# Kernel optimization log

Hardware: AMD Instinct MI355X
Metric: run time of the kernel (lower is better)

## Reference

```python
import jax, jax.numpy as jnp
import numpy as np

K = 2
BN_EPS = 1e-5


def setup_inputs() -> dict:
    key = jax.random.key(0)
    k1, k2, k3 = jax.random.split(key, 3)
    B, C, H, W, D, O = 4, 128, 32, 32, 32, 128
    x = jax.random.normal(k1, (B, C, H, W, D), dtype=jnp.float32)
    conv_w = jax.random.normal(k2, (O, 2 * C), dtype=jnp.float32) * 0.02  # 1x1x1 conv kernel
    conv_b = jax.random.normal(k3, (O,), dtype=jnp.float32) * 0.02
    bn_gamma = jnp.ones((O,), dtype=jnp.float32)
    bn_beta = jnp.zeros((O,), dtype=jnp.float32)
    return {"x": x, "conv_w": conv_w, "conv_b": conv_b,
            "bn_gamma": bn_gamma, "bn_beta": bn_beta}


def _axis_running_max(x, x_j, axis, dim):
    # torch.cat([x[..., -i:], x[..., :-i]], axis) == jnp.roll(x, i, axis)
    shifts = jnp.arange(K, dim, K)

    def step(carry, s):
        diff = x - jnp.roll(x, s, axis=axis)
        return jnp.maximum(carry, diff), None

    x_j, _ = jax.lax.scan(step, x_j, shifts)
    return x_j


def reference(x, conv_w, conv_b, bn_gamma, bn_beta):
    B, C, H, W, D = x.shape
    x_j = jnp.zeros_like(x)
    x_j = _axis_running_max(x, x_j, 2, H)
    x_j = _axis_running_max(x, x_j, 3, W)
    x_j = _axis_running_max(x, x_j, 4, D)
    x_j = jax.lax.stop_gradient(x_j)  # original detaches every x_j update

    xc = jnp.concatenate([x, x_j], axis=1)  # [B, 2C, H, W, D]
    # 1x1x1 Conv3d == per-voxel channel GEMM
    y = jnp.einsum('bchwd,oc->bohwd', xc, conv_w) + conv_b[None, :, None, None, None]

    # BatchNorm3d, training mode (batch statistics over B,H,W,D)
    mean = y.mean(axis=(0, 2, 3, 4), keepdims=True)
    var = ((y - mean) ** 2).mean(axis=(0, 2, 3, 4), keepdims=True)
    yn = (y - mean) * jax.lax.rsqrt(var + BN_EPS)
    yn = yn * bn_gamma[None, :, None, None, None] + bn_beta[None, :, None, None, None]

    # torch nn.GELU default is exact erf form
    return jax.nn.gelu(yn, approximate=False)
```

## Files before the change

kernel.cpp:

```cpp
#include <hip/hip_runtime.h>
#include <hip/hip_bf16.h>

#define BB 4
#define CCH 128
#define C2 256
#define OO 128
#define NVOX 32768
#define NTOT (BB*NVOX)
#define NGB 1024

typedef __attribute__((ext_vector_type(4))) float f32x4;
typedef __attribute__((ext_vector_type(8))) short s16x8;
typedef __attribute__((ext_vector_type(4))) unsigned int u32x4;
typedef unsigned int u32;
typedef unsigned short u16;

#define SWZ(r) ((((r)>>3) ^ (r)) & 7)

__device__ __forceinline__ float bf2f(short s){
  union { u32 i; float f; } cv; cv.i = ((u32)(u16)s) << 16; return cv.f;
}
__device__ __forceinline__ short f2bf(float f){
  union { __hip_bfloat16 h; short s; } cv; cv.h = __float2bfloat16(f); return cv.s;
}
__device__ __forceinline__ u32 pack2(float a, float b){
  return ((u32)(u16)f2bf(a)) | (((u32)(u16)f2bf(b)) << 16);
}
__device__ __forceinline__ float ulo(u32 r){
  union { u32 i; float f; } cv; cv.i = r << 16; return cv.f;
}
__device__ __forceinline__ float uhi(u32 r){
  union { u32 i; float f; } cv; cv.i = r & 0xffff0000u; return cv.f;
}
__device__ __forceinline__ float bfr(float f){ return bf2f(f2bf(f)); }

__global__ __launch_bounds__(256) void k_convw(const float* __restrict__ w, short* __restrict__ wb){
  int i = blockIdx.x*256 + threadIdx.x;
  wb[i] = f2bf(w[i]);
}

__global__ __launch_bounds__(1024) void k_tab(const float* __restrict__ x,
                                              u32* __restrict__ tw, u32* __restrict__ th){
  int t = threadIdx.x;
  u32 bc = blockIdx.x;
  const float* __restrict__ src = x + (size_t)bc*NVOX;
  int a = t >> 5, d = t & 31;
  {
    float m1[2] = {1e30f,1e30f}, m2[2] = {1e30f,1e30f};
    #pragma unroll
    for(int w=0;w<32;w++){
      float v = bfr(src[a*1024 + w*32 + d]);
      int p = w & 1;
      m2[p] = fminf(m2[p], fmaxf(m1[p], v));
      m1[p] = fminf(m1[p], v);
    }
    u32* r = tw + (size_t)bc*2048 + a*64;
    r[d]      = pack2(m1[0], m2[0]);
    r[32 + d] = pack2(m1[1], m2[1]);
  }
  {
    float m1[2] = {1e30f,1e30f}, m2[2] = {1e30f,1e30f};
    #pragma unroll
    for(int h=0;h<32;h++){
      float v = bfr(src[h*1024 + a*32 + d]);
      int p = h & 1;
      m2[p] = fminf(m2[p], fmaxf(m1[p], v));
      m1[p] = fminf(m1[p], v);
    }
    u32* r = th + (size_t)bc*2048 + a*32;
    r[d]        = pack2(m1[0], m2[0]);
    r[1024 + d] = pack2(m1[1], m2[1]);
  }
}

__global__ __launch_bounds__(256) void k_gemm(const float* __restrict__ x, const short* __restrict__ wb,
                                              const u32* __restrict__ tw, const u32* __restrict__ th,
                                              short* __restrict__ y, float* __restrict__ part){
  __shared__ __align__(16) char lds[65536];
  char* ldsJ = lds + 32768;
  u32 blk = blockIdx.x;
  u32 vblk = blk & 255, b = blk >> 8;
  u32 vbase = vblk * 128;
  const float* __restrict__ xb = x + (size_t)b*CCH*NVOX + vbase;
  int t = threadIdx.x;
  int wave = t >> 6, lane = t & 63;
  int wr = wave >> 1, wc = wave & 1;
  int l15 = lane & 15, l4 = lane >> 4;

  {
    int v0   = (t & 15) * 8;
    int line = (t & 15) >> 2;
    int d0   = (t & 3) * 8;
    int cb2  = 2 * (t >> 4);
    int h  = vbase >> 10;
    int w  = ((vbase >> 5) & 31) + line;
    #pragma unroll
    for(int q=0;q<4;q++){
      int c = cb2 + 32*q;
      const float* pe = xb + (size_t)c*NVOX + v0;
      const float* po = pe + NVOX;
      f32x4 e0 = *(const f32x4*)(pe),     e1 = *(const f32x4*)(pe + 4);
      f32x4 o0 = *(const f32x4*)(po),     o1 = *(const f32x4*)(po + 4);
      u32 pr[8];
      #pragma unroll
      for(int e=0;e<4;e++){
        pr[e]   = pack2(e0[e], o0[e]);
        pr[4+e] = pack2(e1[e], o1[e]);
      }
      #pragma unroll
      for(int e=0;e<8;e++){
        int v = v0 + e;
        *(u32*)(lds + v*256 + ((((c>>3) ^ SWZ(v))<<4) | ((c&7)<<1))) = pr[e];
      }
      float m1e[2]={1e30f,1e30f}, m2e[2]={1e30f,1e30f};
      float m1o[2]={1e30f,1e30f}, m2o[2]={1e30f,1e30f};
      #pragma unroll
      for(int e=0;e<8;e++){
        int p = e & 1;
        float xe = ulo(pr[e]), xo = uhi(pr[e]);
        m2e[p] = fminf(m2e[p], fmaxf(m1e[p], xe)); m1e[p] = fminf(m1e[p], xe);
        m2o[p] = fminf(m2o[p], fmaxf(m1o[p], xo)); m1o[p] = fminf(m1o[p], xo);
      }
      #pragma unroll
      for(int mk=1;mk<=2;mk<<=1){
        #pragma unroll
        for(int p=0;p<2;p++){
          float b1, b2;
          b1 = __shfl_xor(m1e[p], mk); b2 = __shfl_xor(m2e[p], mk);
          m2e[p] = fminf(fmaxf(m1e[p], b1), fminf(m2e[p], b2));
          m1e[p] = fminf(m1e[p], b1);
          b1 = __shfl_xor(m1o[p], mk); b2 = __shfl_xor(m2o[p], mk);
          m2o[p] = fminf(fmaxf(m1o[p], b1), fminf(m2o[p], b2));
          m1o[p] = fminf(m1o[p], b1);
        }
      }
      size_t bce = ((size_t)b*CCH + c)*2048;
      const u32* twE = tw + bce + h*64 + (w&1)*32 + d0;
      const u32* thE = th + bce + (h&1)*1024 + w*32 + d0;
      u32x4 we0 = *(const u32x4*)(twE),        we1 = *(const u32x4*)(twE + 4);
      u32x4 wo0 = *(const u32x4*)(twE + 2048), wo1 = *(const u32x4*)(twE + 2052);
      u32x4 he0 = *(const u32x4*)(thE),        he1 = *(const u32x4*)(thE + 4);
      u32x4 ho0 = *(const u32x4*)(thE + 2048), ho1 = *(const u32x4*)(thE + 2052);
      #pragma unroll
      for(int e=0;e<8;e++){
        int p = e & 1;
        float xe = ulo(pr[e]), xo = uhi(pr[e]);
        u32 we = (e<4) ? we0[e] : we1[e-4];
        u32 wo = (e<4) ? wo0[e] : wo1[e-4];
        u32 he = (e<4) ? he0[e] : he1[e-4];
        u32 ho = (e<4) ? ho0[e] : ho1[e-4];
        float mDe = (xe == m1e[p]) ? m2e[p] : m1e[p];
        float mDo = (xo == m1o[p]) ? m2o[p] : m1o[p];
        float w1e = ulo(we); float mWe = (xe == w1e) ? uhi(we) : w1e;
        float w1o = ulo(wo); float mWo = (xo == w1o) ? uhi(wo) : w1o;
        float h1e = ulo(he); float mHe = (xe == h1e) ? uhi(he) : h1e;
        float h1o = ulo(ho); float mHo = (xo == h1o) ? uhi(ho) : h1o;
        float je = fmaxf(0.f, xe - fminf(mDe, fminf(mWe, mHe)));
        float jo = fmaxf(0.f, xo - fminf(mDo, fminf(mWo, mHo)));
        int v = v0 + e;
        *(u32*)(ldsJ + v*256 + ((((c>>3) ^ SWZ(v))<<4) | ((c&7)<<1))) = pack2(je, jo);
      }
    }
  }
  __syncthreads();

  f32x4 acc[4][4];
  #pragma unroll
  for(int mt=0;mt<4;mt++)
    #pragma unroll
    for(int nt=0;nt<4;nt++) acc[mt][nt] = (f32x4){0.f,0.f,0.f,0.f};
  #pragma unroll
  for(int kc=0;kc<2;kc++){
    const char* tile = (kc == 0) ? lds : ldsJ;
    #pragma unroll
    for(int ks=0;ks<4;ks++){
      int kk = ks*32 + l4*8;
      s16x8 afrag[4], bfrag[4];
      #pragma unroll
      for(int nt=0;nt<4;nt++){
        int vloc = wc*64 + nt*16 + l15;
        bfrag[nt] = *(const s16x8*)(tile + vloc*256 + (((kk>>3) ^ SWZ(vloc))<<4));
      }
      #pragma unroll
      for(int mt=0;mt<4;mt++){
        int o = wr*64 + mt*16 + l15;
        afrag[mt] = *(const s16x8*)(wb + o*C2 + kc*128 + kk);
      }
      #pragma unroll
      for(int mt=0;mt<4;mt++)
        #pragma unroll
        for(int nt=0;nt<4;nt++)
          acc[mt][nt] = __builtin_amdgcn_mfma_f32_16x16x32_bf16(afrag[mt], bfrag[nt], acc[mt][nt], 0,0,0);
    }
  }

  __syncthreads();
  #pragma unroll
  for(int mt=0;mt<4;mt++){
    #pragma unroll
    for(int nt=0;nt<4;nt++){
      int vcol = wc*64 + nt*16 + l15;
      #pragma unroll
      for(int r=0;r<4;r++){
        int o = wr*64 + mt*16 + l4*4 + r;
        *(short*)(lds + o*256 + ((((vcol>>3) ^ SWZ(o))<<4) | ((vcol&7)<<1))) = f2bf(acc[mt][nt][r]);
      }
    }
  }
  __syncthreads();
  short* __restrict__ yb = y + (size_t)b*OO*NVOX + vbase;
  #pragma unroll
  for(int q=0;q<8;q++){
    int p = t + q*256;
    int o = p >> 4, vs = (p & 15) * 8;
    s16x8 val = *(const s16x8*)(lds + o*256 + ((((vs>>3) ^ SWZ(o))<<4)));
    *(s16x8*)(yb + (size_t)o*NVOX + vs) = val;
  }

  {
    int o = t >> 1, vh = t & 1;
    float sm = 0.f, ss = 0.f;
    #pragma unroll
    for(int k=0;k<8;k++){
      int vs = vh*64 + k*8;
      s16x8 val = *(const s16x8*)(lds + o*256 + ((((vs>>3) ^ SWZ(o))<<4)));
      #pragma unroll
      for(int e=0;e<8;e++){ float f = bf2f(val[e]); sm += f; ss += f*f; }
    }
    sm += __shfl_xor(sm, 1);
    ss += __shfl_xor(ss, 1);
    if(vh == 0){
      float* pp = part + ((size_t)blk*OO + o)*2;
      pp[0] = sm; pp[1] = ss;
    }
  }
}

__global__ __launch_bounds__(256) void k_statsf(const float* __restrict__ part, float* __restrict__ stats){
  int o = blockIdx.x, t = threadIdx.x;
  float sm = 0.f, ss = 0.f;
  #pragma unroll
  for(int k=0;k<4;k++){
    int blk = t + k*256;
    const float* pp = part + ((size_t)blk*OO + o)*2;
    sm += pp[0]; ss += pp[1];
  }
  __shared__ float rs[256], rss[256];
  rs[t] = sm; rss[t] = ss;
  __syncthreads();
  for(int k=128;k>0;k>>=1){
    if(t<k){ rs[t]+=rs[t+k]; rss[t]+=rss[t+k]; }
    __syncthreads();
  }
  if(t==0){
    float inv = 1.0f/(float)NTOT;
    float mean = rs[0]*inv;
    float var = rss[0]*inv - mean*mean;
    stats[2*o]   = mean;
    stats[2*o+1] = rsqrtf(var + 1e-5f);
  }
}

__global__ __launch_bounds__(256) void k_bngelu(const short* __restrict__ y, const float* __restrict__ stats,
                                                const float* __restrict__ gamma, const float* __restrict__ beta,
                                                float* __restrict__ out){
  size_t base = ((size_t)blockIdx.x*256 + threadIdx.x)*8;
  int o = (int)((base >> 15) & 127);
  float mean = stats[2*o], rstd = stats[2*o+1];
  float g  = gamma[o]*rstd;
  float be = beta[o] - mean*g;
  s16x8 u = *(const s16x8*)(y + base);
  f32x4 r0, r1;
  #pragma unroll
  for(int e=0;e<8;e++){
    float yn = bf2f(u[e])*g + be;
    float ge = 0.5f*yn*(1.0f + erff(yn*0.70710678118654752f));
    if(e<4) r0[e] = ge; else r1[e-4] = ge;
  }
  *(f32x4*)(out + base)     = r0;
  *(f32x4*)(out + base + 4) = r1;
}

extern "C" void kernel_launch(void* const* d_in, const int* in_sizes, int n_in,
                              void* d_out, int out_size, void* d_ws, size_t ws_size,
                              hipStream_t stream) {
  (void)in_sizes; (void)n_in; (void)out_size; (void)ws_size;
  const float* x     = (const float*)d_in[0];
  const float* cw    = (const float*)d_in[1];
  const float* gamma = (const float*)d_in[3];
  const float* beta  = (const float*)d_in[4];
  float* out = (float*)d_out;

  char* ws = (char*)d_ws;
  short* wb    = (short*)ws;
  short* y     = (short*)(ws + 65536);
  float* stats = (float*)(ws + 65536 + (size_t)BB*OO*NVOX*2);
  float* part  = stats + 256;
  u32* tw = (u32*)d_out;
  u32* th = tw + (size_t)512*2048;

  k_convw <<<dim3((OO*C2)/256),     dim3(256), 0, stream>>>(cw, wb);
  k_tab   <<<dim3(BB*CCH),         dim3(1024), 0, stream>>>(x, tw, th);
  k_gemm  <<<dim3(BB*(NVOX/128)),  dim3(256), 0, stream>>>(x, wb, tw, th, y, part);
  k_statsf<<<dim3(OO),             dim3(256), 0, stream>>>(part, stats);
  k_bngelu<<<dim3((NTOT*OO)/2048), dim3(256), 0, stream>>>(y, stats, gamma, beta, out);
}
```

Before: 89.59 us.

## Stage bf16 copy of x in k_tab and remap GEMM blocks per XCD

k_tab now also writes a bf16 copy of x into scratch space in the output buffer, and k_gemm reads that half-size copy instead of the fp32 input, dropping the pack-to-bf16 conversion from the GEMM load path. The GEMM block index is also remapped so blocks landing on the same XCD cover contiguous voxel ranges of one batch, aiming for better L2 locality. The cost is an extra 64MB write in k_tab plus reading it back, in place of the GEMM's 128MB fp32 read. Whether this comes out ahead depends on cache residency between the two kernels.

After: 98.79 us. 10.3% more time.

```diff
diff --git a/kernel.cpp b/kernel.cpp
--- a/kernel.cpp
+++ b/kernel.cpp
@@ -7,7 +7,6 @@
 #define OO 128
 #define NVOX 32768
 #define NTOT (BB*NVOX)
-#define NGB 1024
 
 typedef __attribute__((ext_vector_type(4))) float f32x4;
 typedef __attribute__((ext_vector_type(8))) short s16x8;
@@ -40,7 +39,8 @@
 }
 
 __global__ __launch_bounds__(1024) void k_tab(const float* __restrict__ x,
-                                              u32* __restrict__ tw, u32* __restrict__ th){
+                                              u32* __restrict__ tw, u32* __restrict__ th,
+                                              short* __restrict__ xbf){
   int t = threadIdx.x;
   u32 bc = blockIdx.x;
   const float* __restrict__ src = x + (size_t)bc*NVOX;
@@ -71,17 +71,33 @@
     r[d]        = pack2(m1[0], m2[0]);
     r[1024 + d] = pack2(m1[1], m2[1]);
   }
-}
-
-__global__ __launch_bounds__(256) void k_gemm(const float* __restrict__ x, const short* __restrict__ wb,
+  {
+    const float* pl = src + t*32;
+    u32 xp[16];
+    #pragma unroll
+    for(int g=0;g<8;g++){
+      f32x4 v = *(const f32x4*)(pl + g*4);
+      xp[g*2]   = pack2(v[0], v[1]);
+      xp[g*2+1] = pack2(v[2], v[3]);
+    }
+    short* dst = xbf + (size_t)bc*NVOX + t*32;
+    #pragma unroll
+    for(int g=0;g<4;g++)
+      *(u32x4*)(dst + g*8) = (u32x4){xp[g*4],xp[g*4+1],xp[g*4+2],xp[g*4+3]};
+  }
+}
+
+__global__ __launch_bounds__(256) void k_gemm(const short* __restrict__ xbf, const short* __restrict__ wb,
                                               const u32* __restrict__ tw, const u32* __restrict__ th,
                                               short* __restrict__ y, float* __restrict__ part){
   __shared__ __align__(16) char lds[65536];
   char* ldsJ = lds + 32768;
-  u32 blk = blockIdx.x;
-  u32 vblk = blk & 255, b = blk >> 8;
+  u32 orig = blockIdx.x;
+  u32 xcd = orig & 7, slot = orig >> 3;
+  u32 b    = xcd >> 1;
+  u32 vblk = (xcd & 1)*128 + slot;
+  u32 blk  = b*256 + vblk;
   u32 vbase = vblk * 128;
-  const float* __restrict__ xb = x + (size_t)b*CCH*NVOX + vbase;
   int t = threadIdx.x;
   int wave = t >> 6, lane = t & 63;
   int wr = wave >> 1, wc = wave & 1;
@@ -97,16 +113,13 @@
     #pragma unroll
     for(int q=0;q<4;q++){
       int c = cb2 + 32*q;
-      const float* pe = xb + (size_t)c*NVOX + v0;
-      const float* po = pe + NVOX;
-      f32x4 e0 = *(const f32x4*)(pe),     e1 = *(const f32x4*)(pe + 4);
-      f32x4 o0 = *(const f32x4*)(po),     o1 = *(const f32x4*)(po + 4);
+      const short* pe = xbf + ((size_t)(b*CCH + c))*NVOX + vbase + v0;
+      s16x8 ra = *(const s16x8*)(pe);
+      s16x8 rb = *(const s16x8*)(pe + NVOX);
       u32 pr[8];
       #pragma unroll
-      for(int e=0;e<4;e++){
-        pr[e]   = pack2(e0[e], o0[e]);
-        pr[4+e] = pack2(e1[e], o1[e]);
-      }
+      for(int e=0;e<8;e++)
+        pr[e] = ((u32)(u16)ra[e]) | (((u32)(u16)rb[e]) << 16);
       #pragma unroll
       for(int e=0;e<8;e++){
         int v = v0 + e;
@@ -296,12 +309,13 @@
   short* y     = (short*)(ws + 65536);
   float* stats = (float*)(ws + 65536 + (size_t)BB*OO*NVOX*2);
   float* part  = stats + 256;
-  u32* tw = (u32*)d_out;
-  u32* th = tw + (size_t)512*2048;
+  u32* tw  = (u32*)d_out;
+  u32* th  = tw + (size_t)512*2048;
+  short* xbf = (short*)(th + (size_t)512*2048);
 
   k_convw <<<dim3((OO*C2)/256),     dim3(256), 0, stream>>>(cw, wb);
-  k_tab   <<<dim3(BB*CCH),         dim3(1024), 0, stream>>>(x, tw, th);
-  k_gemm  <<<dim3(BB*(NVOX/128)),  dim3(256), 0, stream>>>(x, wb, tw, th, y, part);
+  k_tab   <<<dim3(BB*CCH),         dim3(1024), 0, stream>>>(x, tw, th, xbf);
+  k_gemm  <<<dim3(BB*(NVOX/128)),  dim3(256), 0, stream>>>(xbf, wb, tw, th, y, part);
   k_statsf<<<dim3(OO),             dim3(256), 0, stream>>>(part, stats);
   k_bngelu<<<dim3((NTOT*OO)/2048), dim3(256), 0, stream>>>(y, stats, gamma, beta, out);
 }
```
